# Kernel tuning notes

Hardware: AMD Instinct MI355X
Metric: run time of the kernel (lower is better)

The kernel has to match this reference:

```python
import jax, jax.numpy as jnp
import numpy as np

GC = 64            # in_channels // 4
GROUPS = GC // 4   # 16 groups, 4 channels per group
BIT = 4
QN, QP = -(2 ** (BIT - 1)), 2 ** (BIT - 1) - 1  # -8, 7


def fake_quant(w, s):
    # 4-bit symmetric fake quantization with straight-through rounding
    r = w / s
    r_ste = r + jax.lax.stop_gradient(jnp.round(r) - r)
    return jnp.clip(r_ste, QN, QP) * s


def qconv(x, w, b, s, padding):
    w_q = fake_quant(w, s)
    y = jax.lax.conv_general_dilated(
        x, w_q, window_strides=(1, 1), padding=padding,
        dimension_numbers=('NCHW', 'OIHW', 'NCHW'),
        feature_group_count=GROUPS)
    return y + b[None, :, None, None]


def setup_inputs() -> dict:
    key = jax.random.key(0)
    ks = jax.random.split(key, 7)
    x = jax.random.normal(ks[0], (64, 256, 64, 64), dtype=jnp.float32)
    # grouped conv weights: [out=gc, in_per_group=4, kh, kw]
    w_hw = jax.random.normal(ks[1], (GC, 4, 3, 3), dtype=jnp.float32) * 0.1
    w_w = jax.random.normal(ks[2], (GC, 4, 1, 11), dtype=jnp.float32) * 0.1
    w_h = jax.random.normal(ks[3], (GC, 4, 11, 1), dtype=jnp.float32) * 0.1
    b_hw = jax.random.normal(ks[4], (GC,), dtype=jnp.float32) * 0.01
    b_w = jax.random.normal(ks[5], (GC,), dtype=jnp.float32) * 0.01
    b_h = jax.random.normal(ks[6], (GC,), dtype=jnp.float32) * 0.01
    # per-conv quant scales (max-abs / Qp)
    s_hw = jnp.max(jnp.abs(w_hw)) / QP
    s_w = jnp.max(jnp.abs(w_w)) / QP
    s_h = jnp.max(jnp.abs(w_h)) / QP
    return {"x": x, "w_hw": w_hw, "b_hw": b_hw, "s_hw": s_hw,
            "w_w": w_w, "b_w": b_w, "s_w": s_w,
            "w_h": w_h, "b_h": b_h, "s_h": s_h}


def reference(x, w_hw, b_hw, s_hw, w_w, b_w, s_w, w_h, b_h, s_h):
    c = x.shape[1]
    id_c = c - 3 * GC  # 64
    x_id = x[:, :id_c]
    x_h = x[:, id_c:id_c + GC]
    x_w = x[:, id_c + GC:id_c + 2 * GC]
    x_hw = x[:, id_c + 2 * GC:]
    y_h = qconv(x_h, w_h, b_h, s_h, [(5, 5), (0, 0)])   # (11,1) kernel, pad (5,0)
    y_w = qconv(x_w, w_w, b_w, s_w, [(0, 0), (5, 5)])   # (1,11) kernel, pad (0,5)
    y_hw = qconv(x_hw, w_hw, b_hw, s_hw, [(1, 1), (1, 1)])  # 3x3, pad 1
    return jnp.concatenate((x_id, y_h, y_w, y_hw), axis=1)
```

## Files before the change

kernel.cpp:

```cpp
#include <hip/hip_runtime.h>

typedef float4 f4;

__device__ __forceinline__ f4 ld4(const float* p) { return *reinterpret_cast<const f4*>(p); }
__device__ __forceinline__ void st4(float* p, f4 v) { *reinterpret_cast<f4*>(p) = v; }

__device__ __forceinline__ float qw(float wv, float s) {
    float r = rintf(wv / s);
    r = fminf(fmaxf(r, -8.f), 7.f);
    float q = r * s;
    return __int_as_float(__builtin_amdgcn_readfirstlane(__float_as_int(q)));
}

__global__ __launch_bounds__(256) void ident_k(const float* __restrict__ x,
                                               float* __restrict__ out) {
    int idx = blockIdx.x * 256 + threadIdx.x;
#pragma unroll
    for (int t = 0; t < 4; t++) {
        int i = idx + t * 1048576;
        int n = i >> 16;
        int rem = i & 65535;
        int off = n * 262144 + rem;
        st4(out + (size_t)off * 4, ld4(x + (size_t)off * 4));
    }
}

__global__ __launch_bounds__(256) void conv_h_k(const float* __restrict__ x,
                                                const float* __restrict__ w,
                                                const float* __restrict__ bias,
                                                const float* __restrict__ sp,
                                                float* __restrict__ out) {
    const float s = sp[0];
    int b = blockIdx.x;
    int n = b >> 5;
    int g = (b >> 1) & 15;
    int strip = b & 1;
    int wave = threadIdx.x >> 6;
    int lane = threadIdx.x & 63;
    int oc = g * 4 + wave;
    int x0 = (lane & 15) << 2;
    int y0 = strip * 32 + (lane >> 4) * 8;

    float wq[4][11];
#pragma unroll
    for (int ic = 0; ic < 4; ic++)
#pragma unroll
        for (int k = 0; k < 11; k++)
            wq[ic][k] = qw(w[(oc * 4 + ic) * 11 + k], s);

    float bz = bias[oc];
    f4 acc[8];
#pragma unroll
    for (int r = 0; r < 8; r++) { acc[r].x = bz; acc[r].y = bz; acc[r].z = bz; acc[r].w = bz; }

    const float* xin = x + n * 1048576 + (64 + g * 4) * 4096;
#pragma unroll
    for (int ic = 0; ic < 4; ic++) {
        const float* pl = xin + ic * 4096;
        f4 row[18];
#pragma unroll
        for (int j = 0; j < 18; j++) {
            int y = y0 - 5 + j;
            if (y >= 0 && y < 64) row[j] = ld4(pl + y * 64 + x0);
            else { row[j].x = 0.f; row[j].y = 0.f; row[j].z = 0.f; row[j].w = 0.f; }
        }
#pragma unroll
        for (int r = 0; r < 8; r++)
#pragma unroll
            for (int k = 0; k < 11; k++) {
                float wv = wq[ic][k];
                acc[r].x = fmaf(wv, row[r + k].x, acc[r].x);
                acc[r].y = fmaf(wv, row[r + k].y, acc[r].y);
                acc[r].z = fmaf(wv, row[r + k].z, acc[r].z);
                acc[r].w = fmaf(wv, row[r + k].w, acc[r].w);
            }
    }
    float* po = out + n * 1048576 + (64 + oc) * 4096 + y0 * 64 + x0;
#pragma unroll
    for (int r = 0; r < 8; r++) st4(po + r * 64, acc[r]);
}

__global__ __launch_bounds__(256) void conv_w_k(const float* __restrict__ x,
                                                const float* __restrict__ w,
                                                const float* __restrict__ bias,
                                                const float* __restrict__ sp,
                                                float* __restrict__ out) {
    const float s = sp[0];
    int b = blockIdx.x;
    int n = b >> 6;
    int g = (b >> 2) & 15;
    int strip = b & 3;
    int wave = threadIdx.x >> 6;
    int lane = threadIdx.x & 63;
    int oc = g * 4 + wave;
    int row = strip * 16 + (lane >> 2);
    int x0 = (lane & 3) << 4;

    float wq[4][11];
#pragma unroll
    for (int ic = 0; ic < 4; ic++)
#pragma unroll
        for (int k = 0; k < 11; k++)
            wq[ic][k] = qw(w[(oc * 4 + ic) * 11 + k], s);

    float bz = bias[oc];
    float acc[16];
#pragma unroll
    for (int p = 0; p < 16; p++) acc[p] = bz;

    const float* xin = x + n * 1048576 + (128 + g * 4) * 4096 + row * 64;
#pragma unroll
    for (int ic = 0; ic < 4; ic++) {
        const float* pl = xin + ic * 4096;
        float buf[32];
#pragma unroll
        for (int t = 0; t < 8; t++) {
            int xb = x0 - 8 + t * 4;
            f4 v;
            if (xb >= 0 && xb < 64) v = ld4(pl + xb);
            else { v.x = 0.f; v.y = 0.f; v.z = 0.f; v.w = 0.f; }
            buf[t * 4 + 0] = v.x; buf[t * 4 + 1] = v.y;
            buf[t * 4 + 2] = v.z; buf[t * 4 + 3] = v.w;
        }
#pragma unroll
        for (int p = 0; p < 16; p++)
#pragma unroll
            for (int k = 0; k < 11; k++)
                acc[p] = fmaf(wq[ic][k], buf[p + 3 + k], acc[p]);
    }
    float* po = out + n * 1048576 + (128 + oc) * 4096 + row * 64 + x0;
#pragma unroll
    for (int t = 0; t < 4; t++) {
        f4 v; v.x = acc[t * 4]; v.y = acc[t * 4 + 1]; v.z = acc[t * 4 + 2]; v.w = acc[t * 4 + 3];
        st4(po + t * 4, v);
    }
}

__global__ __launch_bounds__(256) void conv_hw_k(const float* __restrict__ x,
                                                 const float* __restrict__ w,
                                                 const float* __restrict__ bias,
                                                 const float* __restrict__ sp,
                                                 float* __restrict__ out) {
    const float s = sp[0];
    int b = blockIdx.x;
    int n = b >> 6;
    int g = (b >> 2) & 15;
    int strip = b & 3;
    int wave = threadIdx.x >> 6;
    int lane = threadIdx.x & 63;
    int oc = g * 4 + wave;
    int yp = strip * 16 + (lane >> 3) * 2;
    int x0 = (lane & 7) << 3;

    float wq[4][3][3];
#pragma unroll
    for (int ic = 0; ic < 4; ic++)
#pragma unroll
        for (int ky = 0; ky < 3; ky++)
#pragma unroll
            for (int kx = 0; kx < 3; kx++)
                wq[ic][ky][kx] = qw(w[((oc * 4 + ic) * 3 + ky) * 3 + kx], s);

    float bz = bias[oc];
    float acc[2][8];
#pragma unroll
    for (int r = 0; r < 2; r++)
#pragma unroll
        for (int p = 0; p < 8; p++) acc[r][p] = bz;

    const float* xin = x + n * 1048576 + (192 + g * 4) * 4096;
#pragma unroll
    for (int ic = 0; ic < 4; ic++) {
        const float* pl = xin + ic * 4096;
        float buf[4][16];
#pragma unroll
        for (int jr = 0; jr < 4; jr++) {
            int y = yp - 1 + jr;
            bool yok = (y >= 0 && y < 64);
#pragma unroll
            for (int t = 0; t < 4; t++) {
                int xb = x0 - 4 + t * 4;
                f4 v;
                if (yok && xb >= 0 && xb < 64) v = ld4(pl + y * 64 + xb);
                else { v.x = 0.f; v.y = 0.f; v.z = 0.f; v.w = 0.f; }
                buf[jr][t * 4 + 0] = v.x; buf[jr][t * 4 + 1] = v.y;
                buf[jr][t * 4 + 2] = v.z; buf[jr][t * 4 + 3] = v.w;
            }
        }
#pragma unroll
        for (int r = 0; r < 2; r++)
#pragma unroll
            for (int p = 0; p < 8; p++)
#pragma unroll
                for (int ky = 0; ky < 3; ky++)
#pragma unroll
                    for (int kx = 0; kx < 3; kx++)
                        acc[r][p] = fmaf(wq[ic][ky][kx], buf[r + ky][p + 3 + kx], acc[r][p]);
    }
    float* po = out + n * 1048576 + (192 + oc) * 4096 + yp * 64 + x0;
#pragma unroll
    for (int r = 0; r < 2; r++)
#pragma unroll
        for (int t = 0; t < 2; t++) {
            f4 v;
            v.x = acc[r][t * 4]; v.y = acc[r][t * 4 + 1];
            v.z = acc[r][t * 4 + 2]; v.w = acc[r][t * 4 + 3];
            st4(po + r * 64 + t * 4, v);
        }
}

extern "C" void kernel_launch(void* const* d_in, const int* in_sizes, int n_in,
                              void* d_out, int out_size, void* d_ws, size_t ws_size,
                              hipStream_t stream) {
    const float* x    = (const float*)d_in[0];
    const float* w_hw = (const float*)d_in[1];
    const float* b_hw = (const float*)d_in[2];
    const float* s_hw = (const float*)d_in[3];
    const float* w_w  = (const float*)d_in[4];
    const float* b_w  = (const float*)d_in[5];
    const float* s_w  = (const float*)d_in[6];
    const float* w_h  = (const float*)d_in[7];
    const float* b_h  = (const float*)d_in[8];
    const float* s_h  = (const float*)d_in[9];
    float* out = (float*)d_out;

    ident_k<<<4096, 256, 0, stream>>>(x, out);
    conv_h_k<<<2048, 256, 0, stream>>>(x, w_h, b_h, s_h, out);
    conv_w_k<<<4096, 256, 0, stream>>>(x, w_w, b_w, s_w, out);
    conv_hw_k<<<4096, 256, 0, stream>>>(x, w_hw, b_hw, s_hw, out);
}
```

Baseline: 631.9 us.

## Fuse identity copy and three grouped convs into one launch with nontemporal stores

Replaces four separate kernel launches with a single kernel that dispatches on block index to the identity copy, H-conv, W-conv or 3x3 conv path, removing launch gaps and tail effects between kernels. Outputs and the identity copy use nontemporal loads and stores to reduce cache pollution. Weight quantization is done once per wave with lane-parallel compute and readlane broadcast, and boundary loads use clamped addresses with zero masking instead of branches. The H-conv path streams rows and accumulates as each row arrives, which reduces register pressure. The fused kernel may have higher register usage across branches, which could lower occupancy.

```diff
diff --git a/kernel.cpp b/kernel.cpp
--- a/kernel.cpp
+++ b/kernel.cpp
@@ -1,212 +1,202 @@
 #include <hip/hip_runtime.h>
 
 typedef float4 f4;
+typedef float nf4 __attribute__((ext_vector_type(4)));
 
 __device__ __forceinline__ f4 ld4(const float* p) { return *reinterpret_cast<const f4*>(p); }
-__device__ __forceinline__ void st4(float* p, f4 v) { *reinterpret_cast<f4*>(p) = v; }
-
-__device__ __forceinline__ float qw(float wv, float s) {
-    float r = rintf(wv / s);
-    r = fminf(fmaxf(r, -8.f), 7.f);
-    float q = r * s;
-    return __int_as_float(__builtin_amdgcn_readfirstlane(__float_as_int(q)));
-}
-
-__global__ __launch_bounds__(256) void ident_k(const float* __restrict__ x,
-                                               float* __restrict__ out) {
-    int idx = blockIdx.x * 256 + threadIdx.x;
-#pragma unroll
-    for (int t = 0; t < 4; t++) {
-        int i = idx + t * 1048576;
-        int n = i >> 16;
-        int rem = i & 65535;
-        int off = n * 262144 + rem;
-        st4(out + (size_t)off * 4, ld4(x + (size_t)off * 4));
-    }
-}
-
-__global__ __launch_bounds__(256) void conv_h_k(const float* __restrict__ x,
-                                                const float* __restrict__ w,
-                                                const float* __restrict__ bias,
-                                                const float* __restrict__ sp,
-                                                float* __restrict__ out) {
-    const float s = sp[0];
-    int b = blockIdx.x;
-    int n = b >> 5;
-    int g = (b >> 1) & 15;
-    int strip = b & 1;
+
+__device__ __forceinline__ nf4 ldnt4(const float* p) {
+    return __builtin_nontemporal_load(reinterpret_cast<const nf4*>(p));
+}
+__device__ __forceinline__ void stnt4(float* p, nf4 v) {
+    __builtin_nontemporal_store(v, reinterpret_cast<nf4*>(p));
+}
+
+__device__ __forceinline__ f4 fma4(float w, f4 a, f4 c) {
+    c.x = fmaf(w, a.x, c.x); c.y = fmaf(w, a.y, c.y);
+    c.z = fmaf(w, a.z, c.z); c.w = fmaf(w, a.w, c.w);
+    return c;
+}
+
+template<int NW>
+__device__ __forceinline__ void quant_bcast(const float* __restrict__ wb, float s, float* wq) {
+    int lane = threadIdx.x & 63;
+    float q = 0.f;
+    if (lane < NW) {
+        float r = rintf(wb[lane] / s);
+        r = fminf(fmaxf(r, -8.f), 7.f);
+        q = r * s;
+    }
+#pragma unroll
+    for (int k = 0; k < NW; k++)
+        wq[k] = __int_as_float(__builtin_amdgcn_readlane(__float_as_int(q), k));
+}
+
+__global__ __launch_bounds__(256) void fused_k(
+    const float* __restrict__ x,
+    const float* __restrict__ w_h,  const float* __restrict__ b_h,  const float* __restrict__ s_h,
+    const float* __restrict__ w_w,  const float* __restrict__ b_w,  const float* __restrict__ s_w,
+    const float* __restrict__ w_hw, const float* __restrict__ b_hw, const float* __restrict__ s_hw,
+    float* __restrict__ out)
+{
+    int blk  = blockIdx.x;
     int wave = threadIdx.x >> 6;
     int lane = threadIdx.x & 63;
-    int oc = g * 4 + wave;
-    int x0 = (lane & 15) << 2;
-    int y0 = strip * 32 + (lane >> 4) * 8;
-
-    float wq[4][11];
-#pragma unroll
-    for (int ic = 0; ic < 4; ic++)
-#pragma unroll
-        for (int k = 0; k < 11; k++)
-            wq[ic][k] = qw(w[(oc * 4 + ic) * 11 + k], s);
-
-    float bz = bias[oc];
-    f4 acc[8];
-#pragma unroll
-    for (int r = 0; r < 8; r++) { acc[r].x = bz; acc[r].y = bz; acc[r].z = bz; acc[r].w = bz; }
-
-    const float* xin = x + n * 1048576 + (64 + g * 4) * 4096;
-#pragma unroll
-    for (int ic = 0; ic < 4; ic++) {
-        const float* pl = xin + ic * 4096;
-        f4 row[18];
-#pragma unroll
-        for (int j = 0; j < 18; j++) {
-            int y = y0 - 5 + j;
-            if (y >= 0 && y < 64) row[j] = ld4(pl + y * 64 + x0);
-            else { row[j].x = 0.f; row[j].y = 0.f; row[j].z = 0.f; row[j].w = 0.f; }
-        }
-#pragma unroll
-        for (int r = 0; r < 8; r++)
-#pragma unroll
-            for (int k = 0; k < 11; k++) {
-                float wv = wq[ic][k];
-                acc[r].x = fmaf(wv, row[r + k].x, acc[r].x);
-                acc[r].y = fmaf(wv, row[r + k].y, acc[r].y);
-                acc[r].z = fmaf(wv, row[r + k].z, acc[r].z);
-                acc[r].w = fmaf(wv, row[r + k].w, acc[r].w);
-            }
-    }
-    float* po = out + n * 1048576 + (64 + oc) * 4096 + y0 * 64 + x0;
-#pragma unroll
-    for (int r = 0; r < 8; r++) st4(po + r * 64, acc[r]);
-}
-
-__global__ __launch_bounds__(256) void conv_w_k(const float* __restrict__ x,
-                                                const float* __restrict__ w,
-                                                const float* __restrict__ bias,
-                                                const float* __restrict__ sp,
-                                                float* __restrict__ out) {
-    const float s = sp[0];
-    int b = blockIdx.x;
-    int n = b >> 6;
-    int g = (b >> 2) & 15;
-    int strip = b & 3;
-    int wave = threadIdx.x >> 6;
-    int lane = threadIdx.x & 63;
-    int oc = g * 4 + wave;
-    int row = strip * 16 + (lane >> 2);
-    int x0 = (lane & 3) << 4;
-
-    float wq[4][11];
-#pragma unroll
-    for (int ic = 0; ic < 4; ic++)
-#pragma unroll
-        for (int k = 0; k < 11; k++)
-            wq[ic][k] = qw(w[(oc * 4 + ic) * 11 + k], s);
-
-    float bz = bias[oc];
-    float acc[16];
-#pragma unroll
-    for (int p = 0; p < 16; p++) acc[p] = bz;
-
-    const float* xin = x + n * 1048576 + (128 + g * 4) * 4096 + row * 64;
-#pragma unroll
-    for (int ic = 0; ic < 4; ic++) {
-        const float* pl = xin + ic * 4096;
-        float buf[32];
-#pragma unroll
-        for (int t = 0; t < 8; t++) {
-            int xb = x0 - 8 + t * 4;
-            f4 v;
-            if (xb >= 0 && xb < 64) v = ld4(pl + xb);
-            else { v.x = 0.f; v.y = 0.f; v.z = 0.f; v.w = 0.f; }
-            buf[t * 4 + 0] = v.x; buf[t * 4 + 1] = v.y;
-            buf[t * 4 + 2] = v.z; buf[t * 4 + 3] = v.w;
-        }
-#pragma unroll
-        for (int p = 0; p < 16; p++)
-#pragma unroll
-            for (int k = 0; k < 11; k++)
-                acc[p] = fmaf(wq[ic][k], buf[p + 3 + k], acc[p]);
-    }
-    float* po = out + n * 1048576 + (128 + oc) * 4096 + row * 64 + x0;
-#pragma unroll
-    for (int t = 0; t < 4; t++) {
-        f4 v; v.x = acc[t * 4]; v.y = acc[t * 4 + 1]; v.z = acc[t * 4 + 2]; v.w = acc[t * 4 + 3];
-        st4(po + t * 4, v);
-    }
-}
-
-__global__ __launch_bounds__(256) void conv_hw_k(const float* __restrict__ x,
-                                                 const float* __restrict__ w,
-                                                 const float* __restrict__ bias,
-                                                 const float* __restrict__ sp,
-                                                 float* __restrict__ out) {
-    const float s = sp[0];
-    int b = blockIdx.x;
-    int n = b >> 6;
-    int g = (b >> 2) & 15;
-    int strip = b & 3;
-    int wave = threadIdx.x >> 6;
-    int lane = threadIdx.x & 63;
-    int oc = g * 4 + wave;
-    int yp = strip * 16 + (lane >> 3) * 2;
-    int x0 = (lane & 7) << 3;
-
-    float wq[4][3][3];
-#pragma unroll
-    for (int ic = 0; ic < 4; ic++)
-#pragma unroll
-        for (int ky = 0; ky < 3; ky++)
-#pragma unroll
-            for (int kx = 0; kx < 3; kx++)
-                wq[ic][ky][kx] = qw(w[((oc * 4 + ic) * 3 + ky) * 3 + kx], s);
-
-    float bz = bias[oc];
-    float acc[2][8];
-#pragma unroll
-    for (int r = 0; r < 2; r++)
-#pragma unroll
-        for (int p = 0; p < 8; p++) acc[r][p] = bz;
-
-    const float* xin = x + n * 1048576 + (192 + g * 4) * 4096;
-#pragma unroll
-    for (int ic = 0; ic < 4; ic++) {
-        const float* pl = xin + ic * 4096;
-        float buf[4][16];
-#pragma unroll
-        for (int jr = 0; jr < 4; jr++) {
-            int y = yp - 1 + jr;
-            bool yok = (y >= 0 && y < 64);
-#pragma unroll
-            for (int t = 0; t < 4; t++) {
-                int xb = x0 - 4 + t * 4;
-                f4 v;
-                if (yok && xb >= 0 && xb < 64) v = ld4(pl + y * 64 + xb);
-                else { v.x = 0.f; v.y = 0.f; v.z = 0.f; v.w = 0.f; }
-                buf[jr][t * 4 + 0] = v.x; buf[jr][t * 4 + 1] = v.y;
-                buf[jr][t * 4 + 2] = v.z; buf[jr][t * 4 + 3] = v.w;
-            }
-        }
+
+    if (blk < 4096) {
+        int idx = (blk << 8) + threadIdx.x;
+#pragma unroll
+        for (int t = 0; t < 4; t++) {
+            int i   = idx + t * 1048576;
+            int n   = i >> 16;
+            int rem = i & 65535;
+            size_t off = ((size_t)n * 262144 + rem) * 4;
+            stnt4(out + off, ldnt4(x + off));
+        }
+        return;
+    }
+
+    if (blk < 6144) {
+        int b = blk - 4096;
+        int n = b >> 5, g = (b >> 1) & 15, strip = b & 1;
+        int oc = g * 4 + wave;
+        float wq[44];
+        quant_bcast<44>(w_h + oc * 44, s_h[0], wq);
+        float bz = b_h[oc];
+        int x0 = (lane & 15) << 2;
+        int y0 = strip * 32 + (lane >> 4) * 8;
+
+        f4 acc[8];
+#pragma unroll
+        for (int r = 0; r < 8; r++) { acc[r].x = bz; acc[r].y = bz; acc[r].z = bz; acc[r].w = bz; }
+
+        const float* xin = x + n * 1048576 + (64 + g * 4) * 4096 + x0;
+#pragma unroll
+        for (int ic = 0; ic < 4; ic++) {
+            const float* pl = xin + ic * 4096;
+#pragma unroll
+            for (int j = 0; j < 18; j++) {
+                int y  = y0 - 5 + j;
+                int yc = min(max(y, 0), 63);
+                f4 v = ld4(pl + yc * 64);
+                if (y != yc) { v.x = 0.f; v.y = 0.f; v.z = 0.f; v.w = 0.f; }
+#pragma unroll
+                for (int r = 0; r < 8; r++) {
+                    int k = j - r;
+                    if (k >= 0 && k < 11)
+                        acc[r] = fma4(wq[ic * 11 + k], v, acc[r]);
+                }
+            }
+        }
+        float* po = out + n * 1048576 + (64 + oc) * 4096 + y0 * 64 + x0;
+#pragma unroll
+        for (int r = 0; r < 8; r++) {
+            nf4 v; v.x = acc[r].x; v.y = acc[r].y; v.z = acc[r].z; v.w = acc[r].w;
+            stnt4(po + r * 64, v);
+        }
+        return;
+    }
+
+    if (blk < 10240) {
+        int b = blk - 6144;
+        int n = b >> 6, g = (b >> 2) & 15, strip = b & 3;
+        int oc = g * 4 + wave;
+        float wq[44];
+        quant_bcast<44>(w_w + oc * 44, s_w[0], wq);
+        float bz = b_w[oc];
+        int row = strip * 16 + (lane >> 2);
+        int x0  = (lane & 3) << 4;
+
+        float acc[16];
+#pragma unroll
+        for (int p = 0; p < 16; p++) acc[p] = bz;
+
+        const float* xin = x + n * 1048576 + (128 + g * 4) * 4096 + row * 64;
+#pragma unroll
+        for (int ic = 0; ic < 4; ic++) {
+            const float* pl = xin + ic * 4096;
+            float buf[32];
+#pragma unroll
+            for (int t = 0; t < 8; t++) {
+                int xb = x0 - 8 + t * 4;
+                int xc = min(max(xb, 0), 60);
+                f4 v = ld4(pl + xc);
+                if (xb != xc) { v.x = 0.f; v.y = 0.f; v.z = 0.f; v.w = 0.f; }
+                buf[t * 4 + 0] = v.x; buf[t * 4 + 1] = v.y;
+                buf[t * 4 + 2] = v.z; buf[t * 4 + 3] = v.w;
+            }
+#pragma unroll
+            for (int p = 0; p < 16; p++)
+#pragma unroll
+                for (int k = 0; k < 11; k++)
+                    acc[p] = fmaf(wq[ic * 11 + k], buf[p + 3 + k], acc[p]);
+        }
+        float* po = out + n * 1048576 + (128 + oc) * 4096 + row * 64 + x0;
+#pragma unroll
+        for (int t = 0; t < 4; t++) {
+            nf4 v; v.x = acc[t * 4]; v.y = acc[t * 4 + 1]; v.z = acc[t * 4 + 2]; v.w = acc[t * 4 + 3];
+            stnt4(po + t * 4, v);
+        }
+        return;
+    }
+
+    {
+        int b = blk - 10240;
+        int n = b >> 6, g = (b >> 2) & 15, strip = b & 3;
+        int oc = g * 4 + wave;
+        float wq[36];
+        quant_bcast<36>(w_hw + oc * 36, s_hw[0], wq);
+        float bz = b_hw[oc];
+        int yp = strip * 16 + (lane >> 3) * 2;
+        int x0 = (lane & 7) << 3;
+
+        float acc[2][8];
 #pragma unroll
         for (int r = 0; r < 2; r++)
 #pragma unroll
-            for (int p = 0; p < 8; p++)
-#pragma unroll
-                for (int ky = 0; ky < 3; ky++)
-#pragma unroll
-                    for (int kx = 0; kx < 3; kx++)
-                        acc[r][p] = fmaf(wq[ic][ky][kx], buf[r + ky][p + 3 + kx], acc[r][p]);
-    }
-    float* po = out + n * 1048576 + (192 + oc) * 4096 + yp * 64 + x0;
-#pragma unroll
-    for (int r = 0; r < 2; r++)
-#pragma unroll
-        for (int t = 0; t < 2; t++) {
-            f4 v;
-            v.x = acc[r][t * 4]; v.y = acc[r][t * 4 + 1];
-            v.z = acc[r][t * 4 + 2]; v.w = acc[r][t * 4 + 3];
-            st4(po + r * 64 + t * 4, v);
-        }
+            for (int p = 0; p < 8; p++) acc[r][p] = bz;
+
+        const float* xin = x + n * 1048576 + (192 + g * 4) * 4096;
+#pragma unroll
+        for (int ic = 0; ic < 4; ic++) {
+            const float* pl = xin + ic * 4096;
+            float buf[4][16];
+#pragma unroll
+            for (int jr = 0; jr < 4; jr++) {
+                int y  = yp - 1 + jr;
+                int yc = min(max(y, 0), 63);
+                bool yok = (y == yc);
+#pragma unroll
+                for (int t = 0; t < 4; t++) {
+                    int xb = x0 - 4 + t * 4;
+                    int xc = min(max(xb, 0), 60);
+                    f4 v = ld4(pl + yc * 64 + xc);
+                    if (!yok || xb != xc) { v.x = 0.f; v.y = 0.f; v.z = 0.f; v.w = 0.f; }
+                    buf[jr][t * 4 + 0] = v.x; buf[jr][t * 4 + 1] = v.y;
+                    buf[jr][t * 4 + 2] = v.z; buf[jr][t * 4 + 3] = v.w;
+                }
+            }
+#pragma unroll
+            for (int r = 0; r < 2; r++)
+#pragma unroll
+                for (int p = 0; p < 8; p++)
+#pragma unroll
+                    for (int ky = 0; ky < 3; ky++)
+#pragma unroll
+                        for (int kx = 0; kx < 3; kx++)
+                            acc[r][p] = fmaf(wq[(ic * 3 + ky) * 3 + kx], buf[r + ky][p + 3 + kx], acc[r][p]);
+        }
+        float* po = out + n * 1048576 + (192 + oc) * 4096 + yp * 64 + x0;
+#pragma unroll
+        for (int r = 0; r < 2; r++)
+#pragma unroll
+            for (int t = 0; t < 2; t++) {
+                nf4 v;
+                v.x = acc[r][t * 4]; v.y = acc[r][t * 4 + 1];
+                v.z = acc[r][t * 4 + 2]; v.w = acc[r][t * 4 + 3];
+                stnt4(po + r * 64 + t * 4, v);
+            }
+    }
 }
 
 extern "C" void kernel_launch(void* const* d_in, const int* in_sizes, int n_in,
@@ -224,8 +214,6 @@
     const float* s_h  = (const float*)d_in[9];
     float* out = (float*)d_out;
 
-    ident_k<<<4096, 256, 0, stream>>>(x, out);
-    conv_h_k<<<2048, 256, 0, stream>>>(x, w_h, b_h, s_h, out);
-    conv_w_k<<<4096, 256, 0, stream>>>(x, w_w, b_w, s_w, out);
-    conv_hw_k<<<4096, 256, 0, stream>>>(x, w_hw, b_hw, s_hw, out);
-}
+    fused_k<<<14336, 256, 0, stream>>>(x, w_h, b_h, s_h, w_w, b_w, s_w,
+                                       w_hw, b_hw, s_hw, out);
+}
```

After: 622.7 us. Within noise of the previous version (-1.4%).
